# Kernel tuning notes

Hardware: AMD Instinct MI355X
Metric: run time of the kernel (lower is better)

## Reference

```python
import jax, jax.numpy as jnp
import numpy as np

N = 100000      # nodes
E = 3200000     # edges (avg degree 32)
F_IN = 512
F_OUT = 256


def setup_inputs() -> dict:
    key = jax.random.key(0)
    k1, k2, k3, k4, k5, k6 = jax.random.split(key, 6)
    x = jax.random.normal(k1, (N, F_IN), dtype=jnp.float32)
    row = jax.random.randint(k2, (E,), 0, N)            # destination node of each edge
    col = jax.random.randint(k3, (E,), 0, N)            # source node of each edge
    edge_val = jax.random.uniform(k4, (E,), dtype=jnp.float32)  # normalized adj weights
    stdv = 1.0 / np.sqrt(F_OUT)                         # matches reset_parameters()
    weight = jax.random.uniform(k5, (F_IN, F_OUT), dtype=jnp.float32, minval=-stdv, maxval=stdv)
    bias = jax.random.uniform(k6, (F_OUT,), dtype=jnp.float32, minval=-stdv, maxval=stdv)
    return {"input": x, "weight": weight, "bias": bias, "edge_val": edge_val, "row": row, "col": col}


def reference(input, weight, bias, edge_val, row, col):
    # support = X @ W  (dense projection)
    support = input @ weight                             # [N, F_OUT]
    # SpMM: out[r] += a[r,c] * support[c] over COO edges (torch.spmm(adj, support))
    msgs = edge_val[:, None] * support[col]              # [E, F_OUT] gather + scale
    agg = jax.ops.segment_sum(msgs, row, num_segments=input.shape[0])  # scatter-add
    # np.around(..., decimals=3) applied row-wise in the original
    out = jnp.round(agg * 1000.0) / 1000.0
    return out + bias
```

## Files before the change

kernel.cpp:

```cpp
#include <hip/hip_runtime.h>
#include <hip/hip_bf16.h>

#define N_NODES 100000
#define N_EDGES 3200000
#define FIN 512
#define FOUT 256
#define GEMM_BM 128
#define GEMM_BK 32

#define PSZ 256
#define PSH 8
#define NP 391
#define CAP_LDS 8960
#define SC_CHUNK 16384

typedef __attribute__((ext_vector_type(8))) short short8;
typedef __attribute__((ext_vector_type(4))) float f32x4;

__device__ __forceinline__ unsigned short f2bf(float f) {
    unsigned u = __float_as_uint(f);
    u += 0x7fffu + ((u >> 16) & 1u);
    return (unsigned short)(u >> 16);
}
__device__ __forceinline__ float bf2f(unsigned short h) {
    return __uint_as_float(((unsigned)h) << 16);
}

__device__ __forceinline__ void gload_lds16(const void* g, void* l) {
    __builtin_amdgcn_global_load_lds(
        (const __attribute__((address_space(1))) unsigned*)g,
        (__attribute__((address_space(3))) unsigned*)l, 16, 0, 0);
}

__global__ __launch_bounds__(256) void prep_weight(const float* __restrict__ W,
                                                   unsigned short* __restrict__ Wt) {
    int idx = blockIdx.x * 256 + threadIdx.x;
    if (idx < FIN * FOUT) {
        int k = idx >> 8;
        int n = idx & 255;
        int s = k >> 5;
        int kk = k & 31;
        int kb16 = kk >> 3;
        int u = kb16 ^ (n & 3) ^ ((n >> 2) & 3);
        Wt[(size_t)s * 8192 + n * 32 + u * 8 + (kk & 7)] = f2bf(W[idx]);
    }
}

__global__ __launch_bounds__(512, 2)
void gemm_kernel(const float* __restrict__ X, const unsigned short* __restrict__ Wt,
                 unsigned short* __restrict__ support) {
    __shared__ unsigned short A_lds[GEMM_BM][40];
    __shared__ __align__(16) unsigned short bls[8192];

    const int t = threadIdx.x;
    const int lane = t & 63;
    const int w = t >> 6;
    const int wm = w >> 2;
    const int wn = w & 3;
    const int q = lane >> 4;
    const int lr = lane & 15;
    const int m0 = blockIdx.x * GEMM_BM;

    f32x4 acc[4][4];
#pragma unroll
    for (int i = 0; i < 4; i++)
#pragma unroll
        for (int j = 0; j < 4; j++) acc[i][j] = (f32x4)0.0f;

    const int arow = t >> 2;
    const int acol = (t & 3) * 8;
    const bool avalid = (m0 + arow) < N_NODES;
    const float* Xp = X + (size_t)(m0 + arow) * FIN + acol;

    const unsigned short* gB = Wt + t * 8;
    unsigned short* ldsB0 = &bls[w * 512];
    unsigned short* ldsB1 = &bls[4096 + w * 512];

    for (int s = 0; s < FIN / GEMM_BK; ++s) {
        union { __hip_bfloat162 h[4]; uint4 v; } pk;
        if (avalid) {
            float4 v0 = *(const float4*)(Xp + s * GEMM_BK);
            float4 v1 = *(const float4*)(Xp + s * GEMM_BK + 4);
            pk.h[0] = __float22bfloat162_rn(make_float2(v0.x, v0.y));
            pk.h[1] = __float22bfloat162_rn(make_float2(v0.z, v0.w));
            pk.h[2] = __float22bfloat162_rn(make_float2(v1.x, v1.y));
            pk.h[3] = __float22bfloat162_rn(make_float2(v1.z, v1.w));
        } else {
            pk.v = make_uint4(0, 0, 0, 0);
        }

        __syncthreads();

        gload_lds16(gB + (size_t)s * 8192, ldsB0);
        gload_lds16(gB + (size_t)s * 8192 + 4096, ldsB1);

        *(uint4*)&A_lds[arow][acol] = pk.v;

        __syncthreads();

        short8 af[4], bfr[4];
#pragma unroll
        for (int i = 0; i < 4; i++) af[i] = *(const short8*)&A_lds[wm * 64 + i * 16 + lr][q * 8];
#pragma unroll
        for (int j = 0; j < 4; j++) {
            int nl = wn * 64 + j * 16 + lr;
            int u = q ^ (nl & 3) ^ ((nl >> 2) & 3);
            bfr[j] = *(const short8*)&bls[nl * 32 + u * 8];
        }
#pragma unroll
        for (int i = 0; i < 4; i++)
#pragma unroll
            for (int j = 0; j < 4; j++)
                acc[i][j] = __builtin_amdgcn_mfma_f32_16x16x32_bf16(af[i], bfr[j], acc[i][j], 0, 0, 0);
    }

#pragma unroll
    for (int i = 0; i < 4; i++) {
#pragma unroll
        for (int r = 0; r < 4; r++) {
            int gm = m0 + wm * 64 + i * 16 + q * 4 + r;
            if (gm < N_NODES) {
#pragma unroll
                for (int j = 0; j < 4; j++)
                    support[(size_t)gm * FOUT + wn * 64 + j * 16 + lr] = f2bf(acc[i][j][r]);
            }
        }
    }
}

__global__ __launch_bounds__(256) void part_hist(const int* __restrict__ row,
                                                 unsigned* __restrict__ pcnt) {
    __shared__ unsigned bins[NP];
    for (int i = threadIdx.x; i < NP; i += 256) bins[i] = 0;
    __syncthreads();
    const int e0 = blockIdx.x * 8192;
#pragma unroll
    for (int j = 0; j < 32; ++j) {
        int e = e0 + j * 256 + threadIdx.x;
        if (e < N_EDGES) atomicAdd(&bins[((unsigned)row[e]) >> PSH], 1u);
    }
    __syncthreads();
    for (int i = threadIdx.x; i < NP; i += 256)
        if (bins[i]) atomicAdd(&pcnt[i], bins[i]);
}

__global__ __launch_bounds__(1024) void part_scan(const unsigned* __restrict__ pcnt,
                                                  unsigned* __restrict__ base,
                                                  unsigned* __restrict__ cursor,
                                                  unsigned* __restrict__ row_ptr) {
    __shared__ unsigned s[1024];
    const int t = threadIdx.x;
    unsigned v = (t < NP) ? pcnt[t] : 0u;
    s[t] = v;
    __syncthreads();
#pragma unroll
    for (int off = 1; off < 1024; off <<= 1) {
        unsigned tv = (t >= off) ? s[t - off] : 0u;
        __syncthreads();
        s[t] += tv;
        __syncthreads();
    }
    if (t < NP) {
        unsigned b = s[t] - v;
        base[t] = b;
        cursor[t] = b;
    }
    if (t == 0) {
        base[NP] = N_EDGES;
        row_ptr[N_NODES] = N_EDGES;
    }
}

__global__ __launch_bounds__(256) void part_scatter(const int* __restrict__ row,
                                                    const int* __restrict__ col,
                                                    const float* __restrict__ val,
                                                    unsigned* __restrict__ cursor,
                                                    uint2* __restrict__ part) {
    __shared__ unsigned bins[NP];
    __shared__ unsigned gb[NP];
    for (int i = threadIdx.x; i < NP; i += 256) bins[i] = 0;
    __syncthreads();
    const int e0 = blockIdx.x * SC_CHUNK;
#pragma unroll 4
    for (int j = 0; j < SC_CHUNK / 256; ++j) {
        int e = e0 + j * 256 + threadIdx.x;
        if (e < N_EDGES) atomicAdd(&bins[((unsigned)row[e]) >> PSH], 1u);
    }
    __syncthreads();
    for (int i = threadIdx.x; i < NP; i += 256) {
        unsigned c = bins[i];
        gb[i] = c ? atomicAdd(&cursor[i], c) : 0u;
        bins[i] = 0;
    }
    __syncthreads();
#pragma unroll 4
    for (int j = 0; j < SC_CHUNK / 256; ++j) {
        int e = e0 + j * 256 + threadIdx.x;
        if (e < N_EDGES) {
            unsigned r = (unsigned)row[e];
            unsigned p = r >> PSH;
            unsigned l = atomicAdd(&bins[p], 1u);
            part[gb[p] + l] = make_uint2(((unsigned)col[e]) | ((r & (PSZ - 1u)) << 17),
                                         __float_as_uint(val[e]));
        }
    }
}

__global__ __launch_bounds__(256) void part_finalize(const unsigned* __restrict__ base,
                                                     uint2* __restrict__ part,
                                                     unsigned* __restrict__ row_ptr) {
    __shared__ uint2 recs[CAP_LDS];
    __shared__ unsigned ncnt[PSZ], nsc[PSZ], ccur[PSZ];
    const int p = blockIdx.x;
    const int t = threadIdx.x;
    const unsigned b = base[p];
    unsigned cnt = base[p + 1] - b;
    if (cnt > CAP_LDS) cnt = CAP_LDS;
    ncnt[t] = 0;
    __syncthreads();
    for (unsigned i = t; i < cnt; i += 256) {
        uint2 r = part[b + i];
        recs[i] = r;
        atomicAdd(&ncnt[r.x >> 17], 1u);
    }
    __syncthreads();
    nsc[t] = ncnt[t];
    __syncthreads();
#pragma unroll
    for (int off = 1; off < PSZ; off <<= 1) {
        unsigned tv = (t >= off) ? nsc[t - off] : 0u;
        __syncthreads();
        nsc[t] += tv;
        __syncthreads();
    }
    {
        unsigned ex = nsc[t] - ncnt[t];
        ccur[t] = ex;
        int node = p * PSZ + t;
        if (node < N_NODES) row_ptr[node] = b + ex;
    }
    __syncthreads();
    for (unsigned i = t; i < cnt; i += 256) {
        uint2 r = recs[i];
        unsigned pos = atomicAdd(&ccur[r.x >> 17], 1u);
        part[b + pos] = make_uint2(r.x & 0x1FFFFu, r.y);
    }
}

__global__ __launch_bounds__(256)
void spmm_kernel(const unsigned* __restrict__ row_ptr, const uint2* __restrict__ sorted,
                 const unsigned short* __restrict__ support, const float* __restrict__ bias,
                 float* __restrict__ out, int fb) {
    const int lane = threadIdx.x & 63;
    const int n = blockIdx.x * 4 + (threadIdx.x >> 6);
    const unsigned start = __builtin_amdgcn_readfirstlane(row_ptr[n]);
    const unsigned end   = __builtin_amdgcn_readfirstlane(row_ptr[n + 1]);
    const int fo = fb + lane * 2;
    const unsigned short* sp = support + fo;
    float a0 = 0.f, a1 = 0.f;

    unsigned i = start;
    const unsigned nfull = (end - start) >> 4;
    if (nfull) {
        uint2 e[16];
#pragma unroll
        for (int j = 0; j < 16; ++j) e[j] = sorted[i + j];
        for (unsigned bt = 1; bt < nfull; ++bt) {
            ushort2 s[16];
#pragma unroll
            for (int j = 0; j < 16; ++j) s[j] = *(const ushort2*)(sp + (size_t)e[j].x * FOUT);
            uint2 en[16];
#pragma unroll
            for (int j = 0; j < 16; ++j) en[j] = sorted[i + 16 + j];
#pragma unroll
            for (int j = 0; j < 16; ++j) {
                float v = __uint_as_float(e[j].y);
                a0 += v * bf2f(s[j].x); a1 += v * bf2f(s[j].y);
            }
#pragma unroll
            for (int j = 0; j < 16; ++j) e[j] = en[j];
            i += 16;
        }
        ushort2 s[16];
#pragma unroll
        for (int j = 0; j < 16; ++j) s[j] = *(const ushort2*)(sp + (size_t)e[j].x * FOUT);
#pragma unroll
        for (int j = 0; j < 16; ++j) {
            float v = __uint_as_float(e[j].y);
            a0 += v * bf2f(s[j].x); a1 += v * bf2f(s[j].y);
        }
        i += 16;
    }
    if (end - i >= 8) {
        uint2 e[8];
#pragma unroll
        for (int j = 0; j < 8; ++j) e[j] = sorted[i + j];
        ushort2 s[8];
#pragma unroll
        for (int j = 0; j < 8; ++j) s[j] = *(const ushort2*)(sp + (size_t)e[j].x * FOUT);
#pragma unroll
        for (int j = 0; j < 8; ++j) {
            float v = __uint_as_float(e[j].y);
            a0 += v * bf2f(s[j].x); a1 += v * bf2f(s[j].y);
        }
        i += 8;
    }
    for (; i < end; ++i) {
        uint2 e = sorted[i];
        float v = __uint_as_float(e.y);
        ushort2 s0 = *(const ushort2*)(sp + (size_t)e.x * FOUT);
        a0 += v * bf2f(s0.x); a1 += v * bf2f(s0.y);
    }

    float2 bv = *(const float2*)(bias + fo);
    float2 r;
    r.x = rintf(a0 * 1000.f) * 0.001f + bv.x;
    r.y = rintf(a1 * 1000.f) * 0.001f + bv.y;
    *(float2*)(out + (size_t)n * FOUT + fo) = r;
}

extern "C" void kernel_launch(void* const* d_in, const int* in_sizes, int n_in,
                              void* d_out, int out_size, void* d_ws, size_t ws_size,
                              hipStream_t stream) {
    (void)in_sizes; (void)n_in; (void)out_size; (void)ws_size;
    const float* X    = (const float*)d_in[0];
    const float* W    = (const float*)d_in[1];
    const float* bias = (const float*)d_in[2];
    const float* eval = (const float*)d_in[3];
    const int*   row  = (const int*)d_in[4];
    const int*   col  = (const int*)d_in[5];
    float* out = (float*)d_out;

    char* p = (char*)d_ws;
    auto take = [&](size_t bytes) {
        char* r = p;
        p += (bytes + 511) & ~(size_t)511;
        return r;
    };
    unsigned short* support = (unsigned short*)take((size_t)N_NODES * FOUT * 2);
    unsigned short* Wt      = (unsigned short*)take((size_t)FIN * FOUT * 2);
    unsigned*       pcnt    = (unsigned*)take((size_t)NP * 4);
    unsigned*       base    = (unsigned*)take((size_t)(NP + 1) * 4);
    unsigned*       cursor  = (unsigned*)take((size_t)NP * 4);
    unsigned*       row_ptr = (unsigned*)take((size_t)(N_NODES + 1) * 4);
    uint2*          part    = (uint2*)take((size_t)N_EDGES * 8 + 1024);

    hipMemsetAsync(pcnt, 0, (size_t)NP * 4, stream);
    prep_weight<<<(FIN * FOUT) / 256, 256, 0, stream>>>(W, Wt);
    gemm_kernel<<<(N_NODES + GEMM_BM - 1) / GEMM_BM, 512, 0, stream>>>(X, Wt, support);
    part_hist<<<(N_EDGES + 8191) / 8192, 256, 0, stream>>>(row, pcnt);
    part_scan<<<1, 1024, 0, stream>>>(pcnt, base, cursor, row_ptr);
    part_scatter<<<(N_EDGES + SC_CHUNK - 1) / SC_CHUNK, 256, 0, stream>>>(row, col, eval, cursor, part);
    part_finalize<<<NP, 256, 0, stream>>>(base, part, row_ptr);
    spmm_kernel<<<N_NODES / 4, 256, 0, stream>>>(row_ptr, part, support, bias, out, 0);
    spmm_kernel<<<N_NODES / 4, 256, 0, stream>>>(row_ptr, part, support, bias, out, 128);
}
```

Measured before the change: 702.6 us.

## Replace partitioned two-pass CSR build with per-node global-atomic counting sort

Builds the CSR row pointers with a per-node histogram using global atomics, a three-level prefix scan, and a direct scatter of edges to their final positions with per-node atomic cursors. It removes the partition-level binning and the LDS finalize pass that re-sorted each partition. In exchange it issues millions of scattered global atomics and random stores. The within-row edge order also becomes nondeterministic, which can perturb float sums.

```diff
diff --git a/kernel.cpp b/kernel.cpp
--- a/kernel.cpp
+++ b/kernel.cpp
@@ -8,11 +8,7 @@
 #define GEMM_BM 128
 #define GEMM_BK 32
 
-#define PSZ 256
-#define PSH 8
-#define NP 391
-#define CAP_LDS 8960
-#define SC_CHUNK 16384
+#define SCAN_BLKS 98
 
 typedef __attribute__((ext_vector_type(8))) short short8;
 typedef __attribute__((ext_vector_type(4))) float f32x4;
@@ -128,29 +124,21 @@
     }
 }
 
-__global__ __launch_bounds__(256) void part_hist(const int* __restrict__ row,
-                                                 unsigned* __restrict__ pcnt) {
-    __shared__ unsigned bins[NP];
-    for (int i = threadIdx.x; i < NP; i += 256) bins[i] = 0;
-    __syncthreads();
-    const int e0 = blockIdx.x * 8192;
-#pragma unroll
-    for (int j = 0; j < 32; ++j) {
-        int e = e0 + j * 256 + threadIdx.x;
-        if (e < N_EDGES) atomicAdd(&bins[((unsigned)row[e]) >> PSH], 1u);
-    }
-    __syncthreads();
-    for (int i = threadIdx.x; i < NP; i += 256)
-        if (bins[i]) atomicAdd(&pcnt[i], bins[i]);
-}
-
-__global__ __launch_bounds__(1024) void part_scan(const unsigned* __restrict__ pcnt,
-                                                  unsigned* __restrict__ base,
-                                                  unsigned* __restrict__ cursor,
-                                                  unsigned* __restrict__ row_ptr) {
+__global__ __launch_bounds__(256) void node_hist(const int* __restrict__ row,
+                                                 unsigned* __restrict__ cnt) {
+    int e = blockIdx.x * 2048 + threadIdx.x;
+#pragma unroll
+    for (int j = 0; j < 8; ++j, e += 256)
+        if (e < N_EDGES) atomicAdd(&cnt[row[e]], 1u);
+}
+
+__global__ __launch_bounds__(1024) void scan_l1(const unsigned* __restrict__ cnt,
+                                                unsigned* __restrict__ cursor,
+                                                unsigned* __restrict__ bsum) {
     __shared__ unsigned s[1024];
     const int t = threadIdx.x;
-    unsigned v = (t < NP) ? pcnt[t] : 0u;
+    const int i = blockIdx.x * 1024 + t;
+    unsigned v = (i < N_NODES) ? cnt[i] : 0u;
     s[t] = v;
     __syncthreads();
 #pragma unroll
@@ -160,91 +148,51 @@
         s[t] += tv;
         __syncthreads();
     }
-    if (t < NP) {
-        unsigned b = s[t] - v;
-        base[t] = b;
-        cursor[t] = b;
-    }
-    if (t == 0) {
-        base[NP] = N_EDGES;
-        row_ptr[N_NODES] = N_EDGES;
-    }
-}
-
-__global__ __launch_bounds__(256) void part_scatter(const int* __restrict__ row,
+    if (i < N_NODES) cursor[i] = s[t] - v;
+    if (t == 1023) bsum[blockIdx.x] = s[1023];
+}
+
+__global__ __launch_bounds__(128) void scan_l2(const unsigned* __restrict__ bsum,
+                                               unsigned* __restrict__ boff) {
+    __shared__ unsigned s[128];
+    const int t = threadIdx.x;
+    unsigned v = (t < SCAN_BLKS) ? bsum[t] : 0u;
+    s[t] = v;
+    __syncthreads();
+#pragma unroll
+    for (int off = 1; off < 128; off <<= 1) {
+        unsigned tv = (t >= off) ? s[t - off] : 0u;
+        __syncthreads();
+        s[t] += tv;
+        __syncthreads();
+    }
+    if (t < SCAN_BLKS) boff[t] = s[t] - v;
+}
+
+__global__ __launch_bounds__(1024) void scan_l3(unsigned* __restrict__ cursor,
+                                                const unsigned* __restrict__ boff,
+                                                unsigned* __restrict__ row_ptr) {
+    const int i = blockIdx.x * 1024 + threadIdx.x;
+    if (i < N_NODES) {
+        unsigned v = cursor[i] + boff[blockIdx.x];
+        cursor[i] = v;
+        row_ptr[i] = v;
+    }
+    if (i == 0) row_ptr[N_NODES] = N_EDGES;
+}
+
+__global__ __launch_bounds__(256) void node_scatter(const int* __restrict__ row,
                                                     const int* __restrict__ col,
                                                     const float* __restrict__ val,
                                                     unsigned* __restrict__ cursor,
                                                     uint2* __restrict__ part) {
-    __shared__ unsigned bins[NP];
-    __shared__ unsigned gb[NP];
-    for (int i = threadIdx.x; i < NP; i += 256) bins[i] = 0;
-    __syncthreads();
-    const int e0 = blockIdx.x * SC_CHUNK;
-#pragma unroll 4
-    for (int j = 0; j < SC_CHUNK / 256; ++j) {
-        int e = e0 + j * 256 + threadIdx.x;
-        if (e < N_EDGES) atomicAdd(&bins[((unsigned)row[e]) >> PSH], 1u);
-    }
-    __syncthreads();
-    for (int i = threadIdx.x; i < NP; i += 256) {
-        unsigned c = bins[i];
-        gb[i] = c ? atomicAdd(&cursor[i], c) : 0u;
-        bins[i] = 0;
-    }
-    __syncthreads();
-#pragma unroll 4
-    for (int j = 0; j < SC_CHUNK / 256; ++j) {
-        int e = e0 + j * 256 + threadIdx.x;
+    int e = blockIdx.x * 2048 + threadIdx.x;
+#pragma unroll
+    for (int j = 0; j < 8; ++j, e += 256)
         if (e < N_EDGES) {
-            unsigned r = (unsigned)row[e];
-            unsigned p = r >> PSH;
-            unsigned l = atomicAdd(&bins[p], 1u);
-            part[gb[p] + l] = make_uint2(((unsigned)col[e]) | ((r & (PSZ - 1u)) << 17),
-                                         __float_as_uint(val[e]));
-        }
-    }
-}
-
-__global__ __launch_bounds__(256) void part_finalize(const unsigned* __restrict__ base,
-                                                     uint2* __restrict__ part,
-                                                     unsigned* __restrict__ row_ptr) {
-    __shared__ uint2 recs[CAP_LDS];
-    __shared__ unsigned ncnt[PSZ], nsc[PSZ], ccur[PSZ];
-    const int p = blockIdx.x;
-    const int t = threadIdx.x;
-    const unsigned b = base[p];
-    unsigned cnt = base[p + 1] - b;
-    if (cnt > CAP_LDS) cnt = CAP_LDS;
-    ncnt[t] = 0;
-    __syncthreads();
-    for (unsigned i = t; i < cnt; i += 256) {
-        uint2 r = part[b + i];
-        recs[i] = r;
-        atomicAdd(&ncnt[r.x >> 17], 1u);
-    }
-    __syncthreads();
-    nsc[t] = ncnt[t];
-    __syncthreads();
-#pragma unroll
-    for (int off = 1; off < PSZ; off <<= 1) {
-        unsigned tv = (t >= off) ? nsc[t - off] : 0u;
-        __syncthreads();
-        nsc[t] += tv;
-        __syncthreads();
-    }
-    {
-        unsigned ex = nsc[t] - ncnt[t];
-        ccur[t] = ex;
-        int node = p * PSZ + t;
-        if (node < N_NODES) row_ptr[node] = b + ex;
-    }
-    __syncthreads();
-    for (unsigned i = t; i < cnt; i += 256) {
-        uint2 r = recs[i];
-        unsigned pos = atomicAdd(&ccur[r.x >> 17], 1u);
-        part[b + pos] = make_uint2(r.x & 0x1FFFFu, r.y);
-    }
+            unsigned pos = atomicAdd(&cursor[row[e]], 1u);
+            part[pos] = make_uint2((unsigned)col[e], __float_as_uint(val[e]));
+        }
 }
 
 __global__ __launch_bounds__(256)
@@ -339,19 +287,21 @@
     };
     unsigned short* support = (unsigned short*)take((size_t)N_NODES * FOUT * 2);
     unsigned short* Wt      = (unsigned short*)take((size_t)FIN * FOUT * 2);
-    unsigned*       pcnt    = (unsigned*)take((size_t)NP * 4);
-    unsigned*       base    = (unsigned*)take((size_t)(NP + 1) * 4);
-    unsigned*       cursor  = (unsigned*)take((size_t)NP * 4);
+    unsigned*       cnt     = (unsigned*)take((size_t)N_NODES * 4);
+    unsigned*       cursor  = (unsigned*)take((size_t)N_NODES * 4);
     unsigned*       row_ptr = (unsigned*)take((size_t)(N_NODES + 1) * 4);
+    unsigned*       bsum    = (unsigned*)take((size_t)SCAN_BLKS * 4);
+    unsigned*       boff    = (unsigned*)take((size_t)SCAN_BLKS * 4);
     uint2*          part    = (uint2*)take((size_t)N_EDGES * 8 + 1024);
 
-    hipMemsetAsync(pcnt, 0, (size_t)NP * 4, stream);
+    hipMemsetAsync(cnt, 0, (size_t)N_NODES * 4, stream);
     prep_weight<<<(FIN * FOUT) / 256, 256, 0, stream>>>(W, Wt);
     gemm_kernel<<<(N_NODES + GEMM_BM - 1) / GEMM_BM, 512, 0, stream>>>(X, Wt, support);
-    part_hist<<<(N_EDGES + 8191) / 8192, 256, 0, stream>>>(row, pcnt);
-    part_scan<<<1, 1024, 0, stream>>>(pcnt, base, cursor, row_ptr);
-    part_scatter<<<(N_EDGES + SC_CHUNK - 1) / SC_CHUNK, 256, 0, stream>>>(row, col, eval, cursor, part);
-    part_finalize<<<NP, 256, 0, stream>>>(base, part, row_ptr);
+    node_hist<<<(N_EDGES + 2047) / 2048, 256, 0, stream>>>(row, cnt);
+    scan_l1<<<SCAN_BLKS, 1024, 0, stream>>>(cnt, cursor, bsum);
+    scan_l2<<<1, 128, 0, stream>>>(bsum, boff);
+    scan_l3<<<SCAN_BLKS, 1024, 0, stream>>>(cursor, boff, row_ptr);
+    node_scatter<<<(N_EDGES + 2047) / 2048, 256, 0, stream>>>(row, col, eval, cursor, part);
     spmm_kernel<<<N_NODES / 4, 256, 0, stream>>>(row_ptr, part, support, bias, out, 0);
     spmm_kernel<<<N_NODES / 4, 256, 0, stream>>>(row_ptr, part, support, bias, out, 128);
 }
```

New measurement: 962.8 us. 37.0% more time.
